# Optimization experiments

Measured on AMD Instinct MI355X. Metric: run time of the kernel, lower is better.

## Reference

```python
import jax, jax.numpy as jnp
import numpy as np

N_NODES = 50000
N_EDGES = 800000
IN_CH = 256
H1, D1 = 4, 64   # layer 1: 4 heads x 64 -> 256
H2, D2 = 1, 64   # output layer: 1 head x 64
NEG_SLOPE = 0.2  # DGL GATConv default


def _leaky_relu(x):
    return jnp.where(x >= 0, x, NEG_SLOPE * x)


def gat_conv(h, src, dst, W, attn_l, attn_r, bias, res_W, num_heads, out_feats, apply_elu):
    """DGL GATConv (eval mode, feat_drop=attn_drop=0).
    h: (N, F_in); src/dst: (E,) edge endpoints (edge u->v aggregates at v).
    W: (F_in, H*D); attn_l/attn_r: (H, D); bias: (H*D,); res_W: (F_in, H*D) or None.
    Returns (N, H, D).
    """
    N = h.shape[0]
    ft = (h @ W).reshape(N, num_heads, out_feats)            # (N,H,D)
    el = jnp.sum(ft * attn_l, axis=-1)                        # (N,H)
    er = jnp.sum(ft * attn_r, axis=-1)                        # (N,H)
    e = _leaky_relu(el[src] + er[dst])                        # (E,H)
    # segment softmax over incoming edges of each dst node
    emax = jax.ops.segment_max(e, dst, num_segments=N)        # (N,H)
    emax = jax.lax.stop_gradient(emax)
    ee = jnp.exp(e - emax[dst])                               # (E,H)
    denom = jax.ops.segment_sum(ee, dst, num_segments=N)      # (N,H)
    a = ee / denom[dst]                                       # (E,H)
    msg = ft[src] * a[:, :, None]                             # (E,H,D)
    rst = jax.ops.segment_sum(msg, dst, num_segments=N)       # (N,H,D)
    if res_W is not None:
        rst = rst + (h @ res_W).reshape(N, num_heads, out_feats)
    rst = rst + bias.reshape(num_heads, out_feats)
    if apply_elu:
        rst = jax.nn.elu(rst)
    return rst


def setup_inputs() -> dict:
    key = jax.random.key(0)
    ks = jax.random.split(key, 12)
    feat = jax.random.normal(ks[0], (N_NODES, IN_CH), dtype=jnp.float32)
    src = jax.random.randint(ks[1], (N_EDGES,), 0, N_NODES)
    dst = jax.random.randint(ks[2], (N_EDGES,), 0, N_NODES)
    s = 0.1
    W1 = jax.random.normal(ks[3], (IN_CH, H1 * D1), dtype=jnp.float32) * s
    al1 = jax.random.normal(ks[4], (H1, D1), dtype=jnp.float32) * s
    ar1 = jax.random.normal(ks[5], (H1, D1), dtype=jnp.float32) * s
    b1 = jnp.zeros((H1 * D1,), dtype=jnp.float32)
    W2 = jax.random.normal(ks[6], (H1 * D1, H2 * D2), dtype=jnp.float32) * s
    al2 = jax.random.normal(ks[7], (H2, D2), dtype=jnp.float32) * s
    ar2 = jax.random.normal(ks[8], (H2, D2), dtype=jnp.float32) * s
    b2 = jnp.zeros((H2 * D2,), dtype=jnp.float32)
    resW2 = jax.random.normal(ks[9], (H1 * D1, H2 * D2), dtype=jnp.float32) * s
    return {"feat": feat, "src": src, "dst": dst,
            "W1": W1, "al1": al1, "ar1": ar1, "b1": b1,
            "W2": W2, "al2": al2, "ar2": ar2, "b2": b2, "resW2": resW2}


def reference(feat, src, dst, W1, al1, ar1, b1, W2, al2, ar2, b2, resW2):
    # Layer 1: 4 heads, ELU, no residual (first DGL layer built without residual)
    h = gat_conv(feat, src, dst, W1, al1, ar1, b1, None, H1, D1, True)
    h = h.reshape(N_NODES, H1 * D1)  # flatten(1)
    # Layer 2: 1 head, residual (linear res_fc since 256 != 64), no activation
    h = gat_conv(h, src, dst, W2, al2, ar2, b2, resW2, H2, D2, False)
    return h.mean(axis=1)  # mean over output heads -> (N, out_channels)
```

## Files before the change

### kernel.cpp

```cpp
#include <hip/hip_runtime.h>
#include <math.h>

#define N_NODES 50000
#define N_EDGES 800000
#define ELL_W 64

#define E_SPLIT 400000
#define CONV_BLKS 1792
#define SCAT_BLKS 512

typedef __attribute__((ext_vector_type(8))) short bf16x8;
typedef __attribute__((ext_vector_type(4))) float f32x4;

__device__ __forceinline__ float leaky(float x) { return x >= 0.f ? x : 0.2f * x; }
__device__ __forceinline__ unsigned short f2bf(float f) {
  unsigned u = __float_as_uint(f);
  return (unsigned short)((u + 0x7fffu + ((u >> 16) & 1u)) >> 16);
}
__device__ __forceinline__ float bflo(unsigned u) { return __uint_as_float(u << 16); }
__device__ __forceinline__ float bfhi(unsigned u) { return __uint_as_float(u & 0xffff0000u); }
__device__ __forceinline__ unsigned pack2(float a, float b) {
  return (unsigned)f2bf(a) | ((unsigned)f2bf(b) << 16);
}

__device__ __forceinline__ void scat4(const int* __restrict__ src, const int* __restrict__ dst,
                                      int* __restrict__ cnt, unsigned short* __restrict__ ell,
                                      int e) {
  int4 d4 = *(const int4*)(dst + e);
  int4 s4 = *(const int4*)(src + e);
  int sl;
  sl = atomicAdd(cnt + d4.x, 1);
  if (sl < ELL_W) __builtin_nontemporal_store((unsigned short)s4.x, ell + d4.x * ELL_W + sl);
  sl = atomicAdd(cnt + d4.y, 1);
  if (sl < ELL_W) __builtin_nontemporal_store((unsigned short)s4.y, ell + d4.y * ELL_W + sl);
  sl = atomicAdd(cnt + d4.z, 1);
  if (sl < ELL_W) __builtin_nontemporal_store((unsigned short)s4.z, ell + d4.z * ELL_W + sl);
  sl = atomicAdd(cnt + d4.w, 1);
  if (sl < ELL_W) __builtin_nontemporal_store((unsigned short)s4.w, ell + d4.w * ELL_W + sl);
}

__launch_bounds__(256)
__global__ void prep_k(const float* __restrict__ feat, const float* __restrict__ W1,
                       const float* __restrict__ W2, const float* __restrict__ resW2,
                       short* __restrict__ featb, short* __restrict__ Wt1,
                       short* __restrict__ Wt2, const int* __restrict__ src,
                       const int* __restrict__ dst, int* __restrict__ cnt,
                       unsigned short* __restrict__ ell) {
  if (blockIdx.x >= CONV_BLKS) {
    const int gtid = (blockIdx.x - CONV_BLKS) * 256 + threadIdx.x;
    const int gsz = SCAT_BLKS * 256;
    for (int q = gtid; q < E_SPLIT / 4; q += gsz) scat4(src, dst, cnt, ell, q * 4);
    return;
  }
  const int gtid = blockIdx.x * 256 + threadIdx.x;
  const int gsz = CONV_BLKS * 256;
  for (int idx = gtid; idx < 256 * 256; idx += gsz) {
    int n = idx >> 8, k = idx & 255;
    Wt1[idx] = (short)f2bf(W1[(size_t)k * 256 + n]);
  }
  for (int idx = gtid; idx < 128 * 256; idx += gsz) {
    int n = idx >> 8, k = idx & 255;
    float v = (n < 64) ? W2[(size_t)k * 64 + n] : resW2[(size_t)k * 64 + (n - 64)];
    Wt2[idx] = (short)f2bf(v);
  }
  const float4* f4 = (const float4*)feat;
  uint2* fb2 = (uint2*)featb;
  for (int idx = gtid; idx < N_NODES * 64; idx += gsz) {
    float4 f = f4[idx];
    uint2 o;
    o.x = pack2(f.x, f.y);
    o.y = pack2(f.z, f.w);
    fb2[idx] = o;
  }
}

template <int MODE, bool SCAT>
__launch_bounds__(256)
__global__ void mfma_gemm_k(const short* __restrict__ A, const short* __restrict__ Bt,
                            const float* __restrict__ bias, const float* __restrict__ al,
                            const float* __restrict__ ar, float* __restrict__ elp,
                            float* __restrict__ erp, short* __restrict__ Cb,
                            float* __restrict__ Cf, const int* __restrict__ src,
                            const int* __restrict__ dst, int* __restrict__ cnt,
                            unsigned short* __restrict__ ell, int M, int K, int N) {
  constexpr int EPI_COLS = (MODE == 0) ? 136 : 72;
  union SharedU {
    struct { short As[4][128][8]; short Bs[4][128][8]; } ab;
    short epi[128 * EPI_COLS];
  };
  __shared__ SharedU sh;

  if (SCAT && blockIdx.y == 2) {
    const int gtid = blockIdx.x * 256 + threadIdx.x;
    const int gsz = gridDim.x * 256;
    for (int q = gtid; q < (N_EDGES - E_SPLIT) / 4; q += gsz)
      scat4(src, dst, cnt, ell, E_SPLIT + q * 4);
    return;
  }
  const int tid = threadIdx.x;
  const int bm0 = blockIdx.x * 128, bn0 = blockIdx.y * 128;
  const int wave = tid >> 6, lane = tid & 63;
  const int wm = (wave & 1) * 64, wn = (wave >> 1) * 64;
  const int q = lane >> 4, r16 = lane & 15;
  const int srow = tid >> 1, sk = (tid & 1) * 16, sq = (tid & 1) * 2;
  f32x4 acc[4][4] = {};

  for (int k0 = 0; k0 < K; k0 += 32) {
    {
      uint4 v0 = {0, 0, 0, 0}, v1 = {0, 0, 0, 0};
      if (bm0 + srow < M) {
        const uint4* p = (const uint4*)(A + (size_t)(bm0 + srow) * K + k0 + sk);
        v0 = p[0];
        v1 = p[1];
      }
      *(uint4*)&sh.ab.As[sq][srow][0] = v0;
      *(uint4*)&sh.ab.As[sq + 1][srow][0] = v1;
    }
    {
      const uint4* p = (const uint4*)(Bt + (size_t)(bn0 + srow) * K + k0 + sk);
      *(uint4*)&sh.ab.Bs[sq][srow][0] = p[0];
      *(uint4*)&sh.ab.Bs[sq + 1][srow][0] = p[1];
    }
    __syncthreads();
    bf16x8 af[4], bfr[4];
#pragma unroll
    for (int i = 0; i < 4; ++i) af[i] = *(const bf16x8*)&sh.ab.As[q][wm + i * 16 + r16][0];
#pragma unroll
    for (int j = 0; j < 4; ++j) bfr[j] = *(const bf16x8*)&sh.ab.Bs[q][wn + j * 16 + r16][0];
#pragma unroll
    for (int i = 0; i < 4; ++i)
#pragma unroll
      for (int j = 0; j < 4; ++j)
        acc[i][j] = __builtin_amdgcn_mfma_f32_16x16x32_bf16(af[i], bfr[j], acc[i][j], 0, 0, 0);
    __syncthreads();
  }

  if (MODE == 0 || wn == 0) {
    const int head = (bn0 + wn) >> 6;
    float alv[4], arv[4];
#pragma unroll
    for (int j = 0; j < 4; ++j) {
      alv[j] = al[((MODE == 0) ? head * 64 : 0) + j * 16 + r16];
      arv[j] = ar[((MODE == 0) ? head * 64 : 0) + j * 16 + r16];
    }
#pragma unroll
    for (int i = 0; i < 4; ++i) {
#pragma unroll
      for (int reg = 0; reg < 4; ++reg) {
        float dl = acc[i][0][reg] * alv[0] + acc[i][1][reg] * alv[1] +
                   acc[i][2][reg] * alv[2] + acc[i][3][reg] * alv[3];
        float dr = acc[i][0][reg] * arv[0] + acc[i][1][reg] * arv[1] +
                   acc[i][2][reg] * arv[2] + acc[i][3][reg] * arv[3];
#pragma unroll
        for (int mm = 1; mm < 16; mm <<= 1) {
          dl += __shfl_xor(dl, mm);
          dr += __shfl_xor(dr, mm);
        }
        int row_g = bm0 + wm + i * 16 + q * 4 + reg;
        if (r16 == 0 && row_g < M) {
          if (MODE == 0) {
            elp[(size_t)row_g * 4 + head] = dl;
            erp[(size_t)row_g * 4 + head] = dr;
          } else {
            elp[row_g] = dl;
            erp[row_g] = dr;
          }
        }
      }
    }
  }

  if (MODE == 0) {
#pragma unroll
    for (int i = 0; i < 4; ++i)
#pragma unroll
      for (int reg = 0; reg < 4; ++reg) {
        int row = wm + i * 16 + q * 4 + reg;
#pragma unroll
        for (int j = 0; j < 4; ++j)
          sh.epi[row * EPI_COLS + wn + j * 16 + r16] = (short)f2bf(acc[i][j][reg]);
      }
    __syncthreads();
#pragma unroll
    for (int k = 0; k < 8; ++k) {
      int c = k * 256 + tid;
      int row = c >> 4, cc = c & 15;
      int row_g = bm0 + row;
      if (row_g < M) {
        uint4 v = *(const uint4*)&sh.epi[row * EPI_COLS + cc * 8];
        *(uint4*)(Cb + (size_t)row_g * N + bn0 + cc * 8) = v;
      }
    }
  } else {
    if (wn == 0) {
#pragma unroll
      for (int i = 0; i < 4; ++i)
#pragma unroll
        for (int reg = 0; reg < 4; ++reg) {
          int row = wm + i * 16 + q * 4 + reg;
#pragma unroll
          for (int j = 0; j < 4; ++j)
            sh.epi[row * EPI_COLS + j * 16 + r16] = (short)f2bf(acc[i][j][reg]);
        }
    } else {
#pragma unroll
      for (int i = 0; i < 4; ++i)
#pragma unroll
        for (int reg = 0; reg < 4; ++reg) {
          int row_g = bm0 + wm + i * 16 + q * 4 + reg;
          if (row_g >= M) continue;
#pragma unroll
          for (int j = 0; j < 4; ++j) {
            int col = j * 16 + r16;
            Cf[(size_t)row_g * 64 + col] = acc[i][j][reg] + bias[col];
          }
        }
    }
    __syncthreads();
#pragma unroll
    for (int k = 0; k < 4; ++k) {
      int c = k * 256 + tid;
      int row = c >> 3, cc = c & 7;
      int row_g = bm0 + row;
      if (row_g < M) {
        uint4 v = *(const uint4*)&sh.epi[row * EPI_COLS + cc * 8];
        *(uint4*)(Cb + (size_t)row_g * 64 + cc * 8) = v;
      }
    }
  }
}

__launch_bounds__(256)
__global__ void agg1_k(const unsigned short* __restrict__ ell, const int* __restrict__ cnt,
                       const float* __restrict__ el, const float* __restrict__ er,
                       const short* __restrict__ ft, const float* __restrict__ bias,
                       short* __restrict__ h1) {
  int node = blockIdx.x * 4 + (threadIdx.x >> 6);
  int lane = threadIdx.x & 63;
  if (node >= N_NODES) return;
  int deg = min(cnt[node], ELL_W);
  const unsigned short* row = ell + node * ELL_W;
  int h = lane >> 4;
  float erh = er[(size_t)node * 4 + h];
  float denom = 0.f;
  float4 acc = make_float4(0.f, 0.f, 0.f, 0.f);
  int i = 0;
  for (; i + 8 <= deg; i += 8) {
    int s[8];
#pragma unroll
    for (int k = 0; k < 8; ++k) s[k] = row[i + k];
    float e[8];
    uint2 u[8];
#pragma unroll
    for (int k = 0; k < 8; ++k) e[k] = leaky(el[(size_t)s[k] * 4 + h] + erh);
#pragma unroll
    for (int k = 0; k < 8; ++k) u[k] = *(const uint2*)(ft + (size_t)s[k] * 256 + lane * 4);
    float w[8];
#pragma unroll
    for (int k = 0; k < 8; ++k) w[k] = __expf(e[k]);
#pragma unroll
    for (int k = 0; k < 8; ++k) {
      denom += w[k];
      acc.x += w[k] * bflo(u[k].x);
      acc.y += w[k] * bfhi(u[k].x);
      acc.z += w[k] * bflo(u[k].y);
      acc.w += w[k] * bfhi(u[k].y);
    }
  }
  for (; i + 4 <= deg; i += 4) {
    int s0 = row[i + 0], s1 = row[i + 1], s2 = row[i + 2], s3 = row[i + 3];
    float e0 = leaky(el[(size_t)s0 * 4 + h] + erh);
    float e1 = leaky(el[(size_t)s1 * 4 + h] + erh);
    float e2 = leaky(el[(size_t)s2 * 4 + h] + erh);
    float e3 = leaky(el[(size_t)s3 * 4 + h] + erh);
    uint2 u0 = *(const uint2*)(ft + (size_t)s0 * 256 + lane * 4);
    uint2 u1 = *(const uint2*)(ft + (size_t)s1 * 256 + lane * 4);
    uint2 u2 = *(const uint2*)(ft + (size_t)s2 * 256 + lane * 4);
    uint2 u3 = *(const uint2*)(ft + (size_t)s3 * 256 + lane * 4);
    float w0 = __expf(e0), w1 = __expf(e1), w2 = __expf(e2), w3 = __expf(e3);
    denom += (w0 + w1) + (w2 + w3);
    acc.x += (w0 * bflo(u0.x) + w1 * bflo(u1.x)) + (w2 * bflo(u2.x) + w3 * bflo(u3.x));
    acc.y += (w0 * bfhi(u0.x) + w1 * bfhi(u1.x)) + (w2 * bfhi(u2.x) + w3 * bfhi(u3.x));
    acc.z += (w0 * bflo(u0.y) + w1 * bflo(u1.y)) + (w2 * bflo(u2.y) + w3 * bflo(u3.y));
    acc.w += (w0 * bfhi(u0.y) + w1 * bfhi(u1.y)) + (w2 * bfhi(u2.y) + w3 * bfhi(u3.y));
  }
  for (; i < deg; ++i) {
    int s = row[i];
    float e = leaky(el[(size_t)s * 4 + h] + erh);
    uint2 u = *(const uint2*)(ft + (size_t)s * 256 + lane * 4);
    float w = __expf(e);
    denom += w;
    acc.x += w * bflo(u.x);
    acc.y += w * bfhi(u.x);
    acc.z += w * bflo(u.y);
    acc.w += w * bfhi(u.y);
  }
  float inv = (deg > 0) ? 1.f / denom : 0.f;
  float4 b = *(const float4*)(bias + lane * 4);
  float4 v;
  v.x = acc.x * inv + b.x;
  v.y = acc.y * inv + b.y;
  v.z = acc.z * inv + b.z;
  v.w = acc.w * inv + b.w;
  v.x = v.x > 0.f ? v.x : expm1f(v.x);
  v.y = v.y > 0.f ? v.y : expm1f(v.y);
  v.z = v.z > 0.f ? v.z : expm1f(v.z);
  v.w = v.w > 0.f ? v.w : expm1f(v.w);
  uint2 o;
  o.x = pack2(v.x, v.y);
  o.y = pack2(v.z, v.w);
  *(uint2*)(h1 + (size_t)node * 256 + lane * 4) = o;
}

__launch_bounds__(256)
__global__ void agg2_k(const unsigned short* __restrict__ ell, const int* __restrict__ cnt,
                       const float* __restrict__ el, const float* __restrict__ er,
                       const short* __restrict__ ft, float* __restrict__ out) {
  int node = blockIdx.x * 4 + (threadIdx.x >> 6);
  int lane = threadIdx.x & 63;
  if (node >= N_NODES) return;
  int deg = min(cnt[node], ELL_W);
  const unsigned short* row = ell + node * ELL_W;
  float erd = er[node];
  float denom = 0.f, acc = 0.f;
  int i = 0;
  for (; i + 8 <= deg; i += 8) {
    int s[8];
#pragma unroll
    for (int k = 0; k < 8; ++k) s[k] = row[i + k];
    float e[8], f[8];
#pragma unroll
    for (int k = 0; k < 8; ++k) e[k] = leaky(el[s[k]] + erd);
#pragma unroll
    for (int k = 0; k < 8; ++k)
      f[k] = bflo((unsigned)(unsigned short)ft[(size_t)s[k] * 64 + lane]);
#pragma unroll
    for (int k = 0; k < 8; ++k) {
      float w = __expf(e[k]);
      denom += w;
      acc += w * f[k];
    }
  }
  for (; i < deg; ++i) {
    int s = row[i];
    float e = leaky(el[s] + erd);
    float f = bflo((unsigned)(unsigned short)ft[(size_t)s * 64 + lane]);
    float w = __expf(e);
    denom += w;
    acc += w * f;
  }
  float r = (deg > 0) ? acc / denom : 0.f;
  out[(size_t)node * 64 + lane] += r;
}

extern "C" void kernel_launch(void* const* d_in, const int* in_sizes, int n_in,
                              void* d_out, int out_size, void* d_ws, size_t ws_size,
                              hipStream_t stream) {
  const float* feat  = (const float*)d_in[0];
  const int*   src   = (const int*)d_in[1];
  const int*   dst   = (const int*)d_in[2];
  const float* W1    = (const float*)d_in[3];
  const float* al1   = (const float*)d_in[4];
  const float* ar1   = (const float*)d_in[5];
  const float* b1    = (const float*)d_in[6];
  const float* W2    = (const float*)d_in[7];
  const float* al2   = (const float*)d_in[8];
  const float* ar2   = (const float*)d_in[9];
  const float* b2    = (const float*)d_in[10];
  const float* resW2 = (const float*)d_in[11];
  float* out = (float*)d_out;

  char* p = (char*)d_ws;
  short* featb = (short*)p; p += (size_t)N_NODES * 256 * 2;
  short* ft1b = (short*)p; p += (size_t)N_NODES * 256 * 2;
  short* h1b  = (short*)p; p += (size_t)N_NODES * 256 * 2;
  short* ft2b = (short*)p; p += (size_t)N_NODES * 64 * 2;
  short* Wt1  = (short*)p; p += 256 * 256 * 2;
  short* Wt2  = (short*)p; p += 128 * 256 * 2;
  float* el1  = (float*)p; p += (size_t)N_NODES * 4 * 4;
  float* er1  = (float*)p; p += (size_t)N_NODES * 4 * 4;
  float* el2  = (float*)p; p += (size_t)N_NODES * 4;
  float* er2  = (float*)p; p += (size_t)N_NODES * 4;
  int* cnt    = (int*)p;   p += (size_t)N_NODES * 4;
  unsigned short* ell = (unsigned short*)p; p += (size_t)N_NODES * ELL_W * 2;

  hipMemsetAsync(cnt, 0, (size_t)N_NODES * sizeof(int), stream);

  dim3 blk(256);

  prep_k<<<CONV_BLKS + SCAT_BLKS, blk, 0, stream>>>(feat, W1, W2, resW2, featb, Wt1, Wt2,
                                                    src, dst, cnt, ell);

  mfma_gemm_k<0, true><<<dim3(391, 3), blk, 0, stream>>>(
      featb, Wt1, nullptr, al1, ar1, el1, er1, ft1b, nullptr,
      src, dst, cnt, ell, N_NODES, 256, 256);
  agg1_k<<<12500, blk, 0, stream>>>(ell, cnt, el1, er1, ft1b, b1, h1b);

  mfma_gemm_k<1, false><<<dim3(391, 1), blk, 0, stream>>>(
      h1b, Wt2, b2, al2, ar2, el2, er2, ft2b, out,
      nullptr, nullptr, nullptr, nullptr, N_NODES, 256, 128);
  agg2_k<<<12500, blk, 0, stream>>>(ell, cnt, el2, er2, ft2b, out);
}
```

Measured before the change: 289.7 us.

## Pad atomic counters, schedule scatter blocks first, widen per-lane gathers in aggregation

Counters are spaced 16 ints apart so atomics on neighbouring nodes stop sharing cache lines. The scatter blocks now get the low block indices in both prep and GEMM launches, so the atomic-heavy work is dispatched first. agg1 splits each wave into two halves, each taking alternate edges and loading 16-byte rows. agg2 splits into quarters loading 8-byte rows, and both combine partial sums with cross-lane shuffles. The aim is fewer, wider gather loads and less atomic contention, at the cost of a 16x larger counter memset and extra shuffle reductions.

```diff
diff --git a/kernel.cpp b/kernel.cpp
--- a/kernel.cpp
+++ b/kernel.cpp
@@ -4,6 +4,7 @@
 #define N_NODES 50000
 #define N_EDGES 800000
 #define ELL_W 64
+#define CNT_STRIDE 16
 
 #define E_SPLIT 400000
 #define CONV_BLKS 1792
@@ -29,13 +30,13 @@
   int4 d4 = *(const int4*)(dst + e);
   int4 s4 = *(const int4*)(src + e);
   int sl;
-  sl = atomicAdd(cnt + d4.x, 1);
+  sl = atomicAdd(cnt + d4.x * CNT_STRIDE, 1);
   if (sl < ELL_W) __builtin_nontemporal_store((unsigned short)s4.x, ell + d4.x * ELL_W + sl);
-  sl = atomicAdd(cnt + d4.y, 1);
+  sl = atomicAdd(cnt + d4.y * CNT_STRIDE, 1);
   if (sl < ELL_W) __builtin_nontemporal_store((unsigned short)s4.y, ell + d4.y * ELL_W + sl);
-  sl = atomicAdd(cnt + d4.z, 1);
+  sl = atomicAdd(cnt + d4.z * CNT_STRIDE, 1);
   if (sl < ELL_W) __builtin_nontemporal_store((unsigned short)s4.z, ell + d4.z * ELL_W + sl);
-  sl = atomicAdd(cnt + d4.w, 1);
+  sl = atomicAdd(cnt + d4.w * CNT_STRIDE, 1);
   if (sl < ELL_W) __builtin_nontemporal_store((unsigned short)s4.w, ell + d4.w * ELL_W + sl);
 }
 
@@ -46,13 +47,13 @@
                        short* __restrict__ Wt2, const int* __restrict__ src,
                        const int* __restrict__ dst, int* __restrict__ cnt,
                        unsigned short* __restrict__ ell) {
-  if (blockIdx.x >= CONV_BLKS) {
-    const int gtid = (blockIdx.x - CONV_BLKS) * 256 + threadIdx.x;
+  if (blockIdx.x < SCAT_BLKS) {
+    const int gtid = blockIdx.x * 256 + threadIdx.x;
     const int gsz = SCAT_BLKS * 256;
     for (int q = gtid; q < E_SPLIT / 4; q += gsz) scat4(src, dst, cnt, ell, q * 4);
     return;
   }
-  const int gtid = blockIdx.x * 256 + threadIdx.x;
+  const int gtid = (blockIdx.x - SCAT_BLKS) * 256 + threadIdx.x;
   const int gsz = CONV_BLKS * 256;
   for (int idx = gtid; idx < 256 * 256; idx += gsz) {
     int n = idx >> 8, k = idx & 255;
@@ -90,7 +91,7 @@
   };
   __shared__ SharedU sh;
 
-  if (SCAT && blockIdx.y == 2) {
+  if (SCAT && blockIdx.y == 0) {
     const int gtid = blockIdx.x * 256 + threadIdx.x;
     const int gsz = gridDim.x * 256;
     for (int q = gtid; q < (N_EDGES - E_SPLIT) / 4; q += gsz)
@@ -98,7 +99,8 @@
     return;
   }
   const int tid = threadIdx.x;
-  const int bm0 = blockIdx.x * 128, bn0 = blockIdx.y * 128;
+  const int bm0 = blockIdx.x * 128;
+  const int bn0 = (SCAT ? ((int)blockIdx.y - 1) : (int)blockIdx.y) * 128;
   const int wave = tid >> 6, lane = tid & 63;
   const int wm = (wave & 1) * 64, wn = (wave >> 1) * 64;
   const int q = lane >> 4, r16 = lane & 15;
@@ -238,78 +240,81 @@
   int node = blockIdx.x * 4 + (threadIdx.x >> 6);
   int lane = threadIdx.x & 63;
   if (node >= N_NODES) return;
-  int deg = min(cnt[node], ELL_W);
+  int deg = min(cnt[node * CNT_STRIDE], ELL_W);
   const unsigned short* row = ell + node * ELL_W;
-  int h = lane >> 4;
+  const int half = lane >> 5, l5 = lane & 31, h = l5 >> 3;
   float erh = er[(size_t)node * 4 + h];
   float denom = 0.f;
-  float4 acc = make_float4(0.f, 0.f, 0.f, 0.f);
+  float acc[8] = {0.f, 0.f, 0.f, 0.f, 0.f, 0.f, 0.f, 0.f};
   int i = 0;
   for (; i + 8 <= deg; i += 8) {
-    int s[8];
-#pragma unroll
-    for (int k = 0; k < 8; ++k) s[k] = row[i + k];
-    float e[8];
-    uint2 u[8];
-#pragma unroll
-    for (int k = 0; k < 8; ++k) e[k] = leaky(el[(size_t)s[k] * 4 + h] + erh);
-#pragma unroll
-    for (int k = 0; k < 8; ++k) u[k] = *(const uint2*)(ft + (size_t)s[k] * 256 + lane * 4);
-    float w[8];
-#pragma unroll
-    for (int k = 0; k < 8; ++k) w[k] = __expf(e[k]);
-#pragma unroll
-    for (int k = 0; k < 8; ++k) {
+    int s[4];
+#pragma unroll
+    for (int k = 0; k < 4; ++k) s[k] = row[i + k * 2 + half];
+    float e[4];
+#pragma unroll
+    for (int k = 0; k < 4; ++k) e[k] = leaky(el[(size_t)s[k] * 4 + h] + erh);
+    uint4 u[4];
+#pragma unroll
+    for (int k = 0; k < 4; ++k) u[k] = *(const uint4*)(ft + (size_t)s[k] * 256 + l5 * 8);
+    float w[4];
+#pragma unroll
+    for (int k = 0; k < 4; ++k) w[k] = __expf(e[k]);
+#pragma unroll
+    for (int k = 0; k < 4; ++k) {
       denom += w[k];
-      acc.x += w[k] * bflo(u[k].x);
-      acc.y += w[k] * bfhi(u[k].x);
-      acc.z += w[k] * bflo(u[k].y);
-      acc.w += w[k] * bfhi(u[k].y);
-    }
-  }
-  for (; i + 4 <= deg; i += 4) {
-    int s0 = row[i + 0], s1 = row[i + 1], s2 = row[i + 2], s3 = row[i + 3];
-    float e0 = leaky(el[(size_t)s0 * 4 + h] + erh);
-    float e1 = leaky(el[(size_t)s1 * 4 + h] + erh);
-    float e2 = leaky(el[(size_t)s2 * 4 + h] + erh);
-    float e3 = leaky(el[(size_t)s3 * 4 + h] + erh);
-    uint2 u0 = *(const uint2*)(ft + (size_t)s0 * 256 + lane * 4);
-    uint2 u1 = *(const uint2*)(ft + (size_t)s1 * 256 + lane * 4);
-    uint2 u2 = *(const uint2*)(ft + (size_t)s2 * 256 + lane * 4);
-    uint2 u3 = *(const uint2*)(ft + (size_t)s3 * 256 + lane * 4);
-    float w0 = __expf(e0), w1 = __expf(e1), w2 = __expf(e2), w3 = __expf(e3);
-    denom += (w0 + w1) + (w2 + w3);
-    acc.x += (w0 * bflo(u0.x) + w1 * bflo(u1.x)) + (w2 * bflo(u2.x) + w3 * bflo(u3.x));
-    acc.y += (w0 * bfhi(u0.x) + w1 * bfhi(u1.x)) + (w2 * bfhi(u2.x) + w3 * bfhi(u3.x));
-    acc.z += (w0 * bflo(u0.y) + w1 * bflo(u1.y)) + (w2 * bflo(u2.y) + w3 * bflo(u3.y));
-    acc.w += (w0 * bfhi(u0.y) + w1 * bfhi(u1.y)) + (w2 * bfhi(u2.y) + w3 * bfhi(u3.y));
-  }
-  for (; i < deg; ++i) {
-    int s = row[i];
+      acc[0] += w[k] * bflo(u[k].x);
+      acc[1] += w[k] * bfhi(u[k].x);
+      acc[2] += w[k] * bflo(u[k].y);
+      acc[3] += w[k] * bfhi(u[k].y);
+      acc[4] += w[k] * bflo(u[k].z);
+      acc[5] += w[k] * bfhi(u[k].z);
+      acc[6] += w[k] * bflo(u[k].w);
+      acc[7] += w[k] * bfhi(u[k].w);
+    }
+  }
+  for (; i < deg; i += 2) {
+    int idx = i + half;
+    bool v = idx < deg;
+    int s = v ? (int)row[idx] : (int)row[i];
     float e = leaky(el[(size_t)s * 4 + h] + erh);
-    uint2 u = *(const uint2*)(ft + (size_t)s * 256 + lane * 4);
-    float w = __expf(e);
+    uint4 u = *(const uint4*)(ft + (size_t)s * 256 + l5 * 8);
+    float w = v ? __expf(e) : 0.f;
     denom += w;
-    acc.x += w * bflo(u.x);
-    acc.y += w * bfhi(u.x);
-    acc.z += w * bflo(u.y);
-    acc.w += w * bfhi(u.y);
-  }
-  float inv = (deg > 0) ? 1.f / denom : 0.f;
-  float4 b = *(const float4*)(bias + lane * 4);
-  float4 v;
-  v.x = acc.x * inv + b.x;
-  v.y = acc.y * inv + b.y;
-  v.z = acc.z * inv + b.z;
-  v.w = acc.w * inv + b.w;
-  v.x = v.x > 0.f ? v.x : expm1f(v.x);
-  v.y = v.y > 0.f ? v.y : expm1f(v.y);
-  v.z = v.z > 0.f ? v.z : expm1f(v.z);
-  v.w = v.w > 0.f ? v.w : expm1f(v.w);
-  uint2 o;
-  o.x = pack2(v.x, v.y);
-  o.y = pack2(v.z, v.w);
-  *(uint2*)(h1 + (size_t)node * 256 + lane * 4) = o;
+    acc[0] += w * bflo(u.x);
+    acc[1] += w * bfhi(u.x);
+    acc[2] += w * bflo(u.y);
+    acc[3] += w * bfhi(u.y);
+    acc[4] += w * bflo(u.z);
+    acc[5] += w * bfhi(u.z);
+    acc[6] += w * bflo(u.w);
+    acc[7] += w * bfhi(u.w);
+  }
+  denom += __shfl_xor(denom, 32);
+#pragma unroll
+  for (int k = 0; k < 8; ++k) acc[k] += __shfl_xor(acc[k], 32);
+  if (half == 0) {
+    float inv = (deg > 0) ? 1.f / denom : 0.f;
+    float4 b0 = *(const float4*)(bias + l5 * 8);
+    float4 b1 = *(const float4*)(bias + l5 * 8 + 4);
+    float v[8];
+    v[0] = acc[0] * inv + b0.x;
+    v[1] = acc[1] * inv + b0.y;
+    v[2] = acc[2] * inv + b0.z;
+    v[3] = acc[3] * inv + b0.w;
+    v[4] = acc[4] * inv + b1.x;
+    v[5] = acc[5] * inv + b1.y;
+    v[6] = acc[6] * inv + b1.z;
+    v[7] = acc[7] * inv + b1.w;
+#pragma unroll
+    for (int k = 0; k < 8; ++k) v[k] = v[k] > 0.f ? v[k] : expm1f(v[k]);
+    uint4 o;
+    o.x = pack2(v[0], v[1]);
+    o.y = pack2(v[2], v[3]);
+    o.z = pack2(v[4], v[5]);
+    o.w = pack2(v[6], v[7]);
+    *(uint4*)(h1 + (size_t)node * 256 + l5 * 8) = o;
+  }
 }
 
 __launch_bounds__(256)
@@ -319,38 +324,55 @@
   int node = blockIdx.x * 4 + (threadIdx.x >> 6);
   int lane = threadIdx.x & 63;
   if (node >= N_NODES) return;
-  int deg = min(cnt[node], ELL_W);
+  int deg = min(cnt[node * CNT_STRIDE], ELL_W);
   const unsigned short* row = ell + node * ELL_W;
+  const int qtr = lane >> 4, l4 = lane & 15;
   float erd = er[node];
-  float denom = 0.f, acc = 0.f;
+  float denom = 0.f;
+  float acc[4] = {0.f, 0.f, 0.f, 0.f};
   int i = 0;
   for (; i + 8 <= deg; i += 8) {
-    int s[8];
-#pragma unroll
-    for (int k = 0; k < 8; ++k) s[k] = row[i + k];
-    float e[8], f[8];
-#pragma unroll
-    for (int k = 0; k < 8; ++k) e[k] = leaky(el[s[k]] + erd);
-#pragma unroll
-    for (int k = 0; k < 8; ++k)
-      f[k] = bflo((unsigned)(unsigned short)ft[(size_t)s[k] * 64 + lane]);
-#pragma unroll
-    for (int k = 0; k < 8; ++k) {
-      float w = __expf(e[k]);
-      denom += w;
-      acc += w * f[k];
-    }
-  }
-  for (; i < deg; ++i) {
-    int s = row[i];
+    int s0 = row[i + qtr], s1 = row[i + 4 + qtr];
+    float e0 = leaky(el[s0] + erd), e1 = leaky(el[s1] + erd);
+    uint2 u0 = *(const uint2*)(ft + (size_t)s0 * 64 + l4 * 4);
+    uint2 u1 = *(const uint2*)(ft + (size_t)s1 * 64 + l4 * 4);
+    float w0 = __expf(e0), w1 = __expf(e1);
+    denom += w0 + w1;
+    acc[0] += w0 * bflo(u0.x) + w1 * bflo(u1.x);
+    acc[1] += w0 * bfhi(u0.x) + w1 * bfhi(u1.x);
+    acc[2] += w0 * bflo(u0.y) + w1 * bflo(u1.y);
+    acc[3] += w0 * bfhi(u0.y) + w1 * bfhi(u1.y);
+  }
+  for (; i < deg; i += 4) {
+    int idx = i + qtr;
+    bool v = idx < deg;
+    int s = v ? (int)row[idx] : (int)row[i];
     float e = leaky(el[s] + erd);
-    float f = bflo((unsigned)(unsigned short)ft[(size_t)s * 64 + lane]);
-    float w = __expf(e);
+    uint2 u = *(const uint2*)(ft + (size_t)s * 64 + l4 * 4);
+    float w = v ? __expf(e) : 0.f;
     denom += w;
-    acc += w * f;
-  }
-  float r = (deg > 0) ? acc / denom : 0.f;
-  out[(size_t)node * 64 + lane] += r;
+    acc[0] += w * bflo(u.x);
+    acc[1] += w * bfhi(u.x);
+    acc[2] += w * bflo(u.y);
+    acc[3] += w * bfhi(u.y);
+  }
+  denom += __shfl_xor(denom, 16);
+  denom += __shfl_xor(denom, 32);
+#pragma unroll
+  for (int k = 0; k < 4; ++k) {
+    acc[k] += __shfl_xor(acc[k], 16);
+    acc[k] += __shfl_xor(acc[k], 32);
+  }
+  if (lane < 16) {
+    float inv = (deg > 0) ? 1.f / denom : 0.f;
+    float4* po = (float4*)(out + (size_t)node * 64 + l4 * 4);
+    float4 o = *po;
+    o.x += acc[0] * inv;
+    o.y += acc[1] * inv;
+    o.z += acc[2] * inv;
+    o.w += acc[3] * inv;
+    *po = o;
+  }
 }
 
 extern "C" void kernel_launch(void* const* d_in, const int* in_sizes, int n_in,
@@ -381,14 +403,14 @@
   float* er1  = (float*)p; p += (size_t)N_NODES * 4 * 4;
   float* el2  = (float*)p; p += (size_t)N_NODES * 4;
   float* er2  = (float*)p; p += (size_t)N_NODES * 4;
-  int* cnt    = (int*)p;   p += (size_t)N_NODES * 4;
+  int* cnt    = (int*)p;   p += (size_t)N_NODES * CNT_STRIDE * 4;
   unsigned short* ell = (unsigned short*)p; p += (size_t)N_NODES * ELL_W * 2;
 
-  hipMemsetAsync(cnt, 0, (size_t)N_NODES * sizeof(int), stream);
+  hipMemsetAsync(cnt, 0, (size_t)N_NODES * CNT_STRIDE * sizeof(int), stream);
 
   dim3 blk(256);
 
-  prep_k<<<CONV_BLKS + SCAT_BLKS, blk, 0, stream>>>(feat, W1, W2, resW2, featb, Wt1, Wt2,
+  prep_k<<<SCAT_BLKS + CONV_BLKS, blk, 0, stream>>>(feat, W1, W2, resW2, featb, Wt1, Wt2,
                                                     src, dst, cnt, ell);
 
   mfma_gemm_k<0, true><<<dim3(391, 3), blk, 0, stream>>>(
```

Result: faster. 279.0 us (-3.7%).
